# Kernel tuning notes

Measured on AMD Instinct MI355X. Metric: run time of the kernel, lower is better.

Reference implementation:

```python
import jax, jax.numpy as jnp
import numpy as np

# Dimensions: B batch, NAP/NUE node counts (= permutation_size1/2), DEG fixed degree,
# EAP/EUE edge counts, D1/D2 feature dims, OUT output_dim, S sample_size.
B, NAP, NUE, DEG = 64, 256, 128, 32
EAP, EUE = NAP * DEG, NUE * DEG
D1, D2, OUT, S = 64, 32, 64, 10
LOG2PI = float(np.log(2.0 * np.pi))


def setup_inputs() -> dict:
    ks = jax.random.split(jax.random.key(0), 16)

    def u(k, shape, fan):  # torch init: uniform(-sqrt(3/fan), sqrt(3/fan))
        ini = float(np.sqrt(3.0 / fan))
        return jax.random.uniform(k, shape, jnp.float32, -ini, ini)

    return {
        "A_AP": jax.random.normal(ks[0], (B, D1, NAP), jnp.float32),
        "A_UE": jax.random.normal(ks[1], (B, D1, NUE), jnp.float32),
        "H": jax.random.normal(ks[2], (B, D2, NAP, NUE), jnp.float32),
        "Q1_AP": u(ks[3], (2 * OUT, D1), OUT * 2 * D1),
        "Q2_AP": u(ks[4], (2 * OUT, D1), OUT * 2 * D1),
        "Q1_UE": u(ks[5], (2 * OUT, D1), OUT * 2 * D1),
        "Q2_UE": u(ks[6], (2 * OUT, D1), OUT * 2 * D1),
        "P1_AP": u(ks[7], (2 * OUT, D2), OUT * 2 * D2),
        "P1_UE": u(ks[8], (2 * OUT, D2), OUT * 2 * D2),
        "Att_AP": u(ks[9], (2 * D1, 1), D1 * 2),
        "Att_UE": u(ks[10], (2 * D1, 1), D1 * 2),
        "bn_weight": jnp.ones((2 * OUT,), jnp.float32),
        "bn_bias": jnp.zeros((2 * OUT,), jnp.float32),
        "Graph_AP_reshape": jax.random.randint(ks[11], (B, 2, EAP), 0, NAP),
        "Graph_UE_reshape": jax.random.randint(ks[12], (B, 2, EUE), 0, NUE),
        "GFA_AP": jax.random.randint(ks[13], (B, NAP, DEG), 0, EAP),
        "GFA_UE": jax.random.randint(ks[14], (B, NUE, DEG), 0, EUE),
        "permutation_size1": NAP,
        "permutation_size2": NUE,
        "BATCH_SIZE": B,
    }


def _gather_nodes(A, idx):
    # A: [B, D, N], idx: [B, E] -> [B, E, D]  (replaces the outer-product+diagonal trick)
    return jnp.take_along_axis(A, idx[:, None, :], axis=2).transpose(0, 2, 1)


def _neighbor_sampling(x_i, x_j, att, key):
    # x_i, x_j: [B, E, D]; att: [2D, 1]
    score = jnp.squeeze(jnp.concatenate([x_i, x_j], axis=-1) @ att, -1)  # [B, E]
    alpha = jnp.clip(jax.nn.sigmoid(jax.nn.leaky_relu(score, 0.2)), 0.01, 0.99)
    logits = jnp.log(alpha) - jnp.log1p(-alpha)
    noise = jax.random.logistic(key, alpha.shape, alpha.dtype)
    gate = jax.nn.sigmoid((logits + noise) / 0.1)  # RelaxedBernoulli(temp=0.1).rsample()
    return x_j * gate[..., None], alpha


def _agg_edges(edge_x, gfa):
    # edge_x: [B, E, D]; gfa: [B, N, deg] indices into E -> [B, D, N] (sum over deg)
    b, n, deg = gfa.shape
    g = jnp.take_along_axis(edge_x, gfa.reshape(b, n * deg, 1), axis=1)
    return g.reshape(b, n, deg, -1).sum(2).transpose(0, 2, 1)


def _kl_bern(a, p=0.5):
    # KL(Bernoulli(a) || Bernoulli(p)) summed over edges -> [B]
    return (a * (jnp.log(a) - jnp.log(p)) + (1 - a) * (jnp.log1p(-a) - jnp.log(1 - p))).sum(-1)


def _batchnorm(x, w, b, eps=1e-5):
    # BatchNorm1d (training-mode batch stats) on [B, C, N]
    m = x.mean(axis=(0, 2), keepdims=True)
    v = jnp.mean((x - m) ** 2, axis=(0, 2), keepdims=True)
    return (x - m) / jnp.sqrt(v + eps) * w[None, :, None] + b[None, :, None]


def _info_xz(A_r, key):
    # A_r: [M, 2*OUT]; diag-Gaussian reparam, S samples, KL-ish MC estimate -> [M]
    mean, raw = A_r[:, :OUT], A_r[:, OUT:]
    std = jax.nn.softplus(raw) + 1e-10
    eps = jax.random.normal(key, (S,) + mean.shape, mean.dtype)
    Z = mean + std * eps
    logq = (-0.5 * eps ** 2 - jnp.log(std) - 0.5 * LOG2PI).sum(-1)
    logp = (-0.5 * Z ** 2 - 0.5 * LOG2PI).sum(-1)
    return (logq - logp).mean(0)


def _forward(floats, Graph_AP_reshape, Graph_UE_reshape, GFA_AP, GFA_UE, p1, p2, bs):
    (A_AP, A_UE, H, Q1_AP, Q2_AP, Q1_UE, Q2_UE,
     P1_AP, P1_UE, Att_AP, Att_UE, bn_w, bn_b) = floats
    k1, k2, k3, k4 = jax.random.split(jax.random.key(42), 4)

    xi_ap = _gather_nodes(A_AP, Graph_AP_reshape[:, 1])
    xj_ap = _gather_nodes(A_AP, Graph_AP_reshape[:, 0])
    xi_ue = _gather_nodes(A_UE, Graph_UE_reshape[:, 1])
    xj_ue = _gather_nodes(A_UE, Graph_UE_reshape[:, 0])

    xj_ap, alpha_ap = _neighbor_sampling(xi_ap, xj_ap, Att_AP, k1)
    xj_ue, alpha_ue = _neighbor_sampling(xi_ue, xj_ue, Att_UE, k2)

    Aap = _agg_edges(xj_ap, GFA_AP)  # [B, D1, NAP]
    Aue = _agg_edges(xj_ue, GFA_UE)  # [B, D1, NUE]

    I_AZ_AP = _kl_bern(alpha_ap)
    I_AZ_UE = _kl_bern(alpha_ue)

    ap = (2.0 * jnp.einsum('od,bdn->bon', Q1_AP, Aap)
          + 2.0 * jnp.einsum('od,bd->bo', Q2_AP, Aue.mean(-1))[:, :, None]
          + 0.1 * jnp.einsum('od,bdn->bon', P1_AP, H.mean(-1)))
    ue = (2.0 * jnp.einsum('od,bdn->bon', Q1_UE, Aue)
          + 2.0 * jnp.einsum('od,bd->bo', Q2_UE, Aap.mean(-1))[:, :, None]
          + 0.1 * jnp.einsum('od,bdn->bon', P1_UE, H.mean(-2)))

    ap = _batchnorm(jax.nn.relu(ap), bn_w, bn_b)
    ue = _batchnorm(jax.nn.relu(ue), bn_w, bn_b)

    I_XZ_AP = _info_xz(ap.transpose(0, 2, 1).reshape(bs * p1, 2 * OUT), k3).reshape(bs, p1).sum(-1)
    I_XZ_UE = _info_xz(ue.transpose(0, 2, 1).reshape(bs * p2, 2 * OUT), k4).reshape(bs, p2).sum(-1)

    return ap[:, :OUT], ue[:, :OUT], I_XZ_AP, I_XZ_UE, I_AZ_AP, I_AZ_UE


def reference(A_AP, A_UE, H, Q1_AP, Q2_AP, Q1_UE, Q2_UE, P1_AP, P1_UE,
              Att_AP, Att_UE, bn_weight, bn_bias,
              Graph_AP_reshape, Graph_UE_reshape, GFA_AP, GFA_UE,
              permutation_size1, permutation_size2, BATCH_SIZE):
    floats = (A_AP, A_UE, H, Q1_AP, Q2_AP, Q1_UE, Q2_UE,
              P1_AP, P1_UE, Att_AP, Att_UE, bn_weight, bn_bias)
    return _forward(floats, Graph_AP_reshape, Graph_UE_reshape, GFA_AP, GFA_UE,
                    permutation_size1, permutation_size2, BATCH_SIZE)
```

## Files before the change

kernel.cpp:

```cpp
#include <hip/hip_runtime.h>
#include <math.h>

#define BB   64
#define NAP  256
#define NUE  128
#define DEG  32
#define EAP  (NAP*DEG)
#define EUE  (NUE*DEG)
#define D1   64
#define D2   32
#define OUTC 64
#define CH   128
#define SS   10

#define TINYF 1.17549435e-38f
#define LOG_HALF (-0.69314718f)

constexpr unsigned rotl_c(unsigned v, int s) { return (v << s) | (v >> (32 - s)); }
struct KeyPair { unsigned hi, lo; };
constexpr KeyPair tf_ck(unsigned k0, unsigned k1, unsigned x0, unsigned x1) {
  unsigned ks2 = k0 ^ k1 ^ 0x1BD11BDAu;
  x0 += k0; x1 += k1;
  const int R[20] = {13,15,26,6, 17,29,16,24, 13,15,26,6, 17,29,16,24, 13,15,26,6};
  const unsigned ia[5] = {k1, ks2, k0, k1, ks2};
  const unsigned ib[5] = {ks2, k0, k1, ks2, k0};
  for (int g = 0; g < 5; ++g) {
    for (int j = 0; j < 4; ++j) { x0 += x1; x1 = rotl_c(x1, R[g*4+j]); x1 ^= x0; }
    x0 += ia[g]; x1 += ib[g] + (unsigned)(g + 1);
  }
  return KeyPair{x0, x1};
}
constexpr KeyPair SK1 = tf_ck(0u, 42u, 0u, 0u);
constexpr KeyPair SK2 = tf_ck(0u, 42u, 0u, 1u);
constexpr KeyPair SK3 = tf_ck(0u, 42u, 0u, 2u);
constexpr KeyPair SK4 = tf_ck(0u, 42u, 0u, 3u);

__device__ __forceinline__ unsigned rb32(unsigned k0, unsigned k1, unsigned ctr) {
  const unsigned ks2 = k0 ^ k1 ^ 0x1BD11BDAu;
  unsigned x0 = k0;
  unsigned x1 = ctr + k1;
#define TFR(r) { x0 += x1; x1 = (x1 << r) | (x1 >> (32 - r)); x1 ^= x0; }
  TFR(13) TFR(15) TFR(26) TFR(6)
  x0 += k1;  x1 += ks2 + 1u;
  TFR(17) TFR(29) TFR(16) TFR(24)
  x0 += ks2; x1 += k0 + 2u;
  TFR(13) TFR(15) TFR(26) TFR(6)
  x0 += k0;  x1 += k1 + 3u;
  TFR(17) TFR(29) TFR(16) TFR(24)
  x0 += k1;  x1 += ks2 + 4u;
  TFR(13) TFR(15) TFR(26) TFR(6)
  x0 += ks2; x1 += k0 + 5u;
#undef TFR
  return x0 ^ x1;
}

__device__ __forceinline__ float bits_to_unit(unsigned bits) {
  return __uint_as_float((bits >> 9) | 0x3f800000u) - 1.0f;
}

__device__ __forceinline__ float erfinv_f32(float x) {
  float w = -log1pf(-x * x);
  float p;
  if (w < 5.0f) {
    w = w - 2.5f;
    p = 2.81022636e-08f;
    p = fmaf(p, w, 3.43273939e-07f);
    p = fmaf(p, w, -3.5233877e-06f);
    p = fmaf(p, w, -4.39150654e-06f);
    p = fmaf(p, w, 0.00021858087f);
    p = fmaf(p, w, -0.00125372503f);
    p = fmaf(p, w, -0.00417768164f);
    p = fmaf(p, w, 0.246640727f);
    p = fmaf(p, w, 1.50140941f);
  } else {
    w = sqrtf(w) - 3.0f;
    p = -0.000200214257f;
    p = fmaf(p, w, 0.000100950558f);
    p = fmaf(p, w, 0.00134934322f);
    p = fmaf(p, w, -0.00367342844f);
    p = fmaf(p, w, 0.00573950773f);
    p = fmaf(p, w, -0.0076224613f);
    p = fmaf(p, w, 0.00943887047f);
    p = fmaf(p, w, 1.00167406f);
    p = fmaf(p, w, 2.83297682f);
  }
  return p * x;
}

__device__ __forceinline__ float normal_from_bits(unsigned bits) {
  float f = bits_to_unit(bits);
  const float lo = -0.99999994f;
  float u = fmaxf(lo, fmaf(f, 2.0f, lo));
  return 1.41421354f * erfinv_f32(u);
}

__device__ __forceinline__ float softplus_f(float x) {
  return fmaxf(x, 0.0f) + log1pf(expf(-fabsf(x)));
}

__global__ __launch_bounds__(256) void edge_kernel(
    const float* __restrict__ A_AP, const float* __restrict__ A_UE,
    const int* __restrict__ GAP, const int* __restrict__ GUE,
    const float* __restrict__ AttAP, const float* __restrict__ AttUE,
    float* __restrict__ gAP, float* __restrict__ gUE,
    float* __restrict__ IAZ_AP, float* __restrict__ IAZ_UE,
    float* __restrict__ amAP, float* __restrict__ amUE)
{
  const int side = blockIdx.y;
  const int b = blockIdx.x;
  const int N = side ? NUE : NAP;
  const int E = side ? EUE : EAP;
  const float* A  = (side ? A_UE : A_AP) + (size_t)b * D1 * N;
  const int* G    = (side ? GUE : GAP) + (size_t)b * 2 * E;
  const float* At = side ? AttUE : AttAP;
  float* gate     = (side ? gUE : gAP) + (size_t)b * E;
  float* IAZ      = side ? IAZ_UE : IAZ_AP;
  float* am       = side ? amUE : amAP;
  const unsigned k0 = side ? SK2.hi : SK1.hi;
  const unsigned k1 = side ? SK2.lo : SK1.lo;
  const int t = threadIdx.x;

  if (t < D1) am[b * D1 + t] = 0.f;

  __shared__ float si_s[NAP];
  __shared__ float sj_s[NAP];
  if (t < N) {
    float a0 = 0.f, a1 = 0.f;
    #pragma unroll
    for (int d = 0; d < D1; ++d) {
      float v = A[d * N + t];
      a0 = fmaf(v, At[d], a0);
      a1 = fmaf(v, At[D1 + d], a1);
    }
    si_s[t] = a0; sj_s[t] = a1;
  }
  __syncthreads();

  float klacc = 0.f;
  for (int e = t; e < E; e += 256) {
    const int ii = G[E + e];
    const int jj = G[e];
    float score = si_s[ii] + sj_s[jj];
    float l = (score >= 0.f) ? score : 0.2f * score;
    float sig = 1.f / (1.f + expf(-l));
    float a = fminf(fmaxf(sig, 0.01f), 0.99f);
    float logits = logf(a) - log1pf(-a);
    unsigned bits = rb32(k0, k1, (unsigned)(b * E + e));
    float f = bits_to_unit(bits);
    float u = fmaxf(TINYF, f + TINYF);
    float noise = logf(u) - log1pf(-u);
    float gv = 1.f / (1.f + expf(-((logits + noise) / 0.1f)));
    gate[e] = gv;
    klacc += a * (logf(a) - LOG_HALF) + (1.f - a) * (log1pf(-a) - LOG_HALF);
  }
  #pragma unroll
  for (int m = 32; m; m >>= 1) klacc += __shfl_xor(klacc, m, 64);
  __shared__ float red[4];
  if ((t & 63) == 0) red[t >> 6] = klacc;
  __syncthreads();
  if (t == 0) IAZ[b] = red[0] + red[1] + red[2] + red[3];
}

template<int N, int E>
__global__ __launch_bounds__(256) void agg_kernel(
    const float* __restrict__ A, const int* __restrict__ Graph,
    const float* __restrict__ gate, const int* __restrict__ GFA,
    float* __restrict__ Aout, float* __restrict__ AmeanRaw)
{
  __shared__ float Als[D1 * N];
  const int b = blockIdx.y;
  const int t = threadIdx.x;
  const int wave = t >> 6, lane = t & 63;
  const int n = blockIdx.x * 64 + lane;

  const int* G0 = Graph + (size_t)b * 2 * E;
  const float* gb = gate + (size_t)b * E;
  const int* gfa = GFA + ((size_t)b * N + n) * DEG;
  int jj[DEG]; float gg[DEG];
  #pragma unroll
  for (int k = 0; k < DEG; ++k) {
    int e = gfa[k];
    jj[k] = G0[e];
    gg[k] = gb[e];
  }

  const float* Ab = A + (size_t)b * D1 * N;
  for (int idx = t * 4; idx < D1 * N; idx += 1024)
    *(float4*)(Als + idx) = *(const float4*)(Ab + idx);
  __syncthreads();

  for (int dd = 0; dd < 16; ++dd) {
    const int d = wave * 16 + dd;
    const float* Ar = Als + d * N;
    float acc = 0.f;
    #pragma unroll
    for (int k = 0; k < DEG; ++k) acc = fmaf(gg[k], Ar[jj[k]], acc);
    Aout[((size_t)b * D1 + d) * N + n] = acc;
    float s = acc;
    #pragma unroll
    for (int m = 32; m; m >>= 1) s += __shfl_xor(s, m, 64);
    if (lane == 0) atomicAdd(&AmeanRaw[b * D1 + d], s);
  }
}

__global__ __launch_bounds__(256) void hreduce_kernel(
    const float* __restrict__ H, float* __restrict__ Hm1, float* __restrict__ Hm2)
{
  const int bd = blockIdx.x;
  const float* Hp = H + (size_t)bd * NAP * NUE;
  const int t = threadIdx.x;
  const int tx = t & 31, ty = t >> 5;
  float4 col = {0.f, 0.f, 0.f, 0.f};
  for (int i = ty; i < NAP; i += 8) {
    float4 v = ((const float4*)(Hp + (size_t)i * NUE))[tx];
    col.x += v.x; col.y += v.y; col.z += v.z; col.w += v.w;
    float rs = v.x + v.y + v.z + v.w;
    #pragma unroll
    for (int m = 16; m; m >>= 1) rs += __shfl_xor(rs, m, 64);
    if (tx == 0) Hm1[(size_t)bd * NAP + i] = rs * (1.0f / NUE);
  }
  __shared__ float cp[8 * 128];
  ((float4*)cp)[ty * 32 + tx] = col;
  __syncthreads();
  if (t < 128) {
    float s = 0.f;
    #pragma unroll
    for (int r = 0; r < 8; ++r) s += cp[r * 128 + t];
    Hm2[(size_t)bd * NUE + t] = s * (1.0f / NAP);
  }
}

__global__ __launch_bounds__(128) void qterm_kernel(
    const float* __restrict__ Q2_AP, const float* __restrict__ Q2_UE,
    const float* __restrict__ AapMeanRaw, const float* __restrict__ AueMeanRaw,
    float* __restrict__ qbAP, float* __restrict__ qbUE,
    float* __restrict__ stAP, float* __restrict__ stUE)
{
  const int b = blockIdx.x;
  const int o = threadIdx.x;
  if (b == 0) {
    #pragma unroll
    for (int i = o; i < 2 * CH; i += 128) { stAP[i] = 0.f; stUE[i] = 0.f; }
  }
  float sA = 0.f, sU = 0.f;
  #pragma unroll
  for (int d = 0; d < D1; ++d) {
    float mUE = AueMeanRaw[b * D1 + d] * (1.0f / NUE);
    float mAP = AapMeanRaw[b * D1 + d] * (1.0f / NAP);
    sA = fmaf(Q2_AP[o * D1 + d], mUE, sA);
    sU = fmaf(Q2_UE[o * D1 + d], mAP, sU);
  }
  qbAP[b * CH + o] = 2.f * sA;
  qbUE[b * CH + o] = 2.f * sU;
}

__global__ __launch_bounds__(256) void mix_kernel(
    const float* __restrict__ Aagg, const float* __restrict__ Hm,
    const float* __restrict__ Q1, const float* __restrict__ P1,
    const float* __restrict__ qb, float* __restrict__ pre,
    float* __restrict__ stat, int N)
{
  const int b = blockIdx.z;
  const int ntile = blockIdx.x;
  const int obase = blockIdx.y * 8;
  __shared__ float As2[D1 * 128];
  __shared__ float Hs[D2 * 128];
  const int t = threadIdx.x;
  const float* Ab = Aagg + (size_t)b * D1 * N + ntile * 128;
  for (int idx = t; idx < D1 * 128; idx += 256) {
    int d = idx >> 7, n = idx & 127;
    As2[idx] = Ab[(size_t)d * N + n];
  }
  const float* Hb = Hm + (size_t)b * D2 * N + ntile * 128;
  for (int idx = t; idx < D2 * 128; idx += 256) {
    int c = idx >> 7, n = idx & 127;
    Hs[idx] = Hb[(size_t)c * N + n];
  }
  __syncthreads();
  const int half = t >> 7, n = t & 127;
  #pragma unroll
  for (int oi = 0; oi < 4; ++oi) {
    const int o = obase + half * 4 + oi;
    float acc = 0.f;
    #pragma unroll
    for (int d = 0; d < D1; ++d) acc = fmaf(Q1[o * D1 + d], As2[d * 128 + n], acc);
    float acc2 = 0.f;
    #pragma unroll
    for (int c = 0; c < D2; ++c) acc2 = fmaf(P1[o * D2 + c], Hs[c * 128 + n], acc2);
    float r = 2.f * acc + qb[b * CH + o] + 0.1f * acc2;
    r = fmaxf(r, 0.f);
    pre[((size_t)b * CH + o) * N + ntile * 128 + n] = r;
    float s1 = r, s2 = r * r;
    #pragma unroll
    for (int m = 32; m; m >>= 1) { s1 += __shfl_xor(s1, m, 64); s2 += __shfl_xor(s2, m, 64); }
    if ((t & 63) == 0) { atomicAdd(&stat[o], s1); atomicAdd(&stat[CH + o], s2); }
  }
}

__global__ __launch_bounds__(256) void bnfinal_kernel(
    const float* __restrict__ statAP, const float* __restrict__ statUE,
    const float* __restrict__ bnw, const float* __restrict__ bnb,
    float* __restrict__ ssAP, float* __restrict__ ssUE,
    float* __restrict__ IXZ)
{
  const int t = threadIdx.x;
  if (t < 2 * BB) IXZ[t] = 0.f;
  if (t < CH) {
    const float inv = 1.0f / (BB * NAP);
    float m = statAP[t] * inv;
    float v = statAP[CH + t] * inv - m * m;
    float sc = bnw[t] / sqrtf(v + 1e-5f);
    ssAP[t] = sc; ssAP[CH + t] = bnb[t] - m * sc;
  } else {
    const int o = t - CH;
    const float inv = 1.0f / (BB * NUE);
    float m = statUE[o] * inv;
    float v = statUE[CH + o] * inv - m * m;
    float sc = bnw[o] / sqrtf(v + 1e-5f);
    ssUE[o] = sc; ssUE[CH + o] = bnb[o] - m * sc;
  }
}

__global__ __launch_bounds__(256) void finalize_kernel(
    const float* __restrict__ preAP, const float* __restrict__ preUE,
    const float* __restrict__ ssAP, const float* __restrict__ ssUE,
    float* __restrict__ outAP, float* __restrict__ outUE,
    float* __restrict__ IXZAP, float* __restrict__ IXZUE)
{
  const int side = blockIdx.z;
  const int N = side ? NUE : NAP;
  if ((int)blockIdx.x * 64 >= N) return;
  const float* pre = side ? preUE : preAP;
  const float* ss  = side ? ssUE  : ssAP;
  float* outp      = side ? outUE : outAP;
  float* IXZ       = side ? IXZUE : IXZAP;
  const unsigned k0 = side ? SK4.hi : SK3.hi;
  const unsigned k1 = side ? SK4.lo : SK3.lo;
  const int ROWS = BB * N;

  const int b = blockIdx.y;
  const int lane = threadIdx.x & 63;
  const int og = threadIdx.x >> 6;
  const int n = blockIdx.x * 64 + lane;
  const int row = b * N + n;
  const float* preb = pre + (size_t)b * CH * N;

  float accZ = 0.f, sumlog = 0.f;
  for (int oi = 0; oi < 16; ++oi) {
    const int o = og * 16 + oi;
    float mpre = preb[o * N + n];
    float rraw = preb[(o + 64) * N + n];
    float x0 = fmaf(mpre, ss[o], ss[CH + o]);
    float x1 = fmaf(rraw, ss[o + 64], ss[CH + o + 64]);
    outp[((size_t)b * OUTC + o) * N + n] = x0;
    float stdv = softplus_f(x1) + 1e-10f;
    sumlog += logf(stdv);
    #pragma unroll
    for (int s = 0; s < SS; ++s) {
      unsigned idx = (unsigned)((s * ROWS + row) * 64 + o);
      float eps = normal_from_bits(rb32(k0, k1, idx));
      float Z = fmaf(stdv, eps, x0);
      accZ += 0.5f * (Z * Z - eps * eps);
    }
  }
  __shared__ float pz[4][64];
  __shared__ float pl[4][64];
  pz[og][lane] = accZ; pl[og][lane] = sumlog;
  __syncthreads();
  if (og == 0) {
    float az = pz[0][lane] + pz[1][lane] + pz[2][lane] + pz[3][lane];
    float al = pl[0][lane] + pl[1][lane] + pl[2][lane] + pl[3][lane];
    float rv = az * (1.0f / SS) - al;
    #pragma unroll
    for (int m = 32; m; m >>= 1) rv += __shfl_xor(rv, m, 64);
    if (lane == 0) atomicAdd(&IXZ[b], rv);
  }
}

constexpr size_t OFF_AMEAN_AP = 0;
constexpr size_t OFF_AMEAN_UE = OFF_AMEAN_AP + BB * D1;
constexpr size_t OFF_STAT_AP  = OFF_AMEAN_UE + BB * D1;
constexpr size_t OFF_STAT_UE  = OFF_STAT_AP + 2 * CH;
constexpr size_t OFF_GATE_AP  = OFF_STAT_UE + 2 * CH;
constexpr size_t OFF_GATE_UE  = OFF_GATE_AP + (size_t)BB * EAP;
constexpr size_t OFF_AAP      = OFF_GATE_UE + (size_t)BB * EUE;
constexpr size_t OFF_AUE      = OFF_AAP + (size_t)BB * D1 * NAP;
constexpr size_t OFF_HM1      = OFF_AUE + (size_t)BB * D1 * NUE;
constexpr size_t OFF_HM2      = OFF_HM1 + (size_t)BB * D2 * NAP;
constexpr size_t OFF_PRE_AP   = OFF_HM2 + (size_t)BB * D2 * NUE;
constexpr size_t OFF_PRE_UE   = OFF_PRE_AP + (size_t)BB * CH * NAP;
constexpr size_t OFF_QB_AP    = OFF_PRE_UE + (size_t)BB * CH * NUE;
constexpr size_t OFF_QB_UE    = OFF_QB_AP + BB * CH;
constexpr size_t OFF_SS_AP    = OFF_QB_UE + BB * CH;
constexpr size_t OFF_SS_UE    = OFF_SS_AP + 2 * CH;
constexpr size_t WS_FLOATS    = OFF_SS_UE + 2 * CH;

extern "C" void kernel_launch(void* const* d_in, const int* in_sizes, int n_in,
                              void* d_out, int out_size, void* d_ws, size_t ws_size,
                              hipStream_t stream)
{
  const float* A_AP  = (const float*)d_in[0];
  const float* A_UE  = (const float*)d_in[1];
  const float* H     = (const float*)d_in[2];
  const float* Q1_AP = (const float*)d_in[3];
  const float* Q2_AP = (const float*)d_in[4];
  const float* Q1_UE = (const float*)d_in[5];
  const float* Q2_UE = (const float*)d_in[6];
  const float* P1_AP = (const float*)d_in[7];
  const float* P1_UE = (const float*)d_in[8];
  const float* AttAP = (const float*)d_in[9];
  const float* AttUE = (const float*)d_in[10];
  const float* bnw   = (const float*)d_in[11];
  const float* bnb   = (const float*)d_in[12];
  const int* GraphAP = (const int*)d_in[13];
  const int* GraphUE = (const int*)d_in[14];
  const int* GFA_AP  = (const int*)d_in[15];
  const int* GFA_UE  = (const int*)d_in[16];

  float* ws = (float*)d_ws;
  if (ws_size < WS_FLOATS * sizeof(float)) return;

  float* amAP  = ws + OFF_AMEAN_AP;
  float* amUE  = ws + OFF_AMEAN_UE;
  float* stAP  = ws + OFF_STAT_AP;
  float* stUE  = ws + OFF_STAT_UE;
  float* gAP   = ws + OFF_GATE_AP;
  float* gUE   = ws + OFF_GATE_UE;
  float* Aap   = ws + OFF_AAP;
  float* Aue   = ws + OFF_AUE;
  float* Hm1   = ws + OFF_HM1;
  float* Hm2   = ws + OFF_HM2;
  float* preAP = ws + OFF_PRE_AP;
  float* preUE = ws + OFF_PRE_UE;
  float* qbAP  = ws + OFF_QB_AP;
  float* qbUE  = ws + OFF_QB_UE;
  float* ssAP  = ws + OFF_SS_AP;
  float* ssUE  = ws + OFF_SS_UE;

  float* out     = (float*)d_out;
  float* outAP   = out;
  float* outUE   = out + (size_t)BB * OUTC * NAP;
  float* IXZ_AP  = out + (size_t)BB * OUTC * (NAP + NUE);
  float* IXZ_UE  = IXZ_AP + BB;
  float* IAZ_AP  = IXZ_UE + BB;
  float* IAZ_UE  = IAZ_AP + BB;

  edge_kernel<<<dim3(BB, 2), 256, 0, stream>>>(
      A_AP, A_UE, GraphAP, GraphUE, AttAP, AttUE,
      gAP, gUE, IAZ_AP, IAZ_UE, amAP, amUE);

  hreduce_kernel<<<BB * D2, 256, 0, stream>>>(H, Hm1, Hm2);

  agg_kernel<NAP, EAP><<<dim3(NAP / 64, BB), 256, 0, stream>>>(
      A_AP, GraphAP, gAP, GFA_AP, Aap, amAP);
  agg_kernel<NUE, EUE><<<dim3(NUE / 64, BB), 256, 0, stream>>>(
      A_UE, GraphUE, gUE, GFA_UE, Aue, amUE);

  qterm_kernel<<<BB, 128, 0, stream>>>(Q2_AP, Q2_UE, amAP, amUE, qbAP, qbUE, stAP, stUE);

  mix_kernel<<<dim3(NAP / 128, 16, BB), 256, 0, stream>>>(
      Aap, Hm1, Q1_AP, P1_AP, qbAP, preAP, stAP, NAP);
  mix_kernel<<<dim3(NUE / 128, 16, BB), 256, 0, stream>>>(
      Aue, Hm2, Q1_UE, P1_UE, qbUE, preUE, stUE, NUE);

  bnfinal_kernel<<<1, 256, 0, stream>>>(stAP, stUE, bnw, bnb, ssAP, ssUE, IXZ_AP);

  finalize_kernel<<<dim3(NAP / 64, BB, 2), 256, 0, stream>>>(
      preAP, preUE, ssAP, ssUE, outAP, outUE, IXZ_AP, IXZ_UE);
}
```

Measured before the change: 778.5 us.

## Merge AP/UE launches and register-tile the mix GEMM over all channels

Fuses the AP and UE agg launches into one grid and likewise for mix, cutting launch count. The mix kernel is restructured so each block covers all 128 output channels for a 64-node tile, with weights staged in padded shared memory and each thread computing an 8x4 register tile. This removes the repeated reloading of A/H tiles across 16 channel-group blocks and the global weight reads, and lowers atomic traffic. It also adds an unroll pragma to the H reduction loop. The cost is higher shared memory and register use per block, which may reduce occupancy.

```diff
diff --git a/kernel.cpp b/kernel.cpp
--- a/kernel.cpp
+++ b/kernel.cpp
@@ -161,21 +161,32 @@
   if (t == 0) IAZ[b] = red[0] + red[1] + red[2] + red[3];
 }
 
-template<int N, int E>
 __global__ __launch_bounds__(256) void agg_kernel(
-    const float* __restrict__ A, const int* __restrict__ Graph,
-    const float* __restrict__ gate, const int* __restrict__ GFA,
-    float* __restrict__ Aout, float* __restrict__ AmeanRaw)
-{
-  __shared__ float Als[D1 * N];
+    const float* __restrict__ A_AP, const float* __restrict__ A_UE,
+    const int* __restrict__ GAP, const int* __restrict__ GUE,
+    const float* __restrict__ gAP, const float* __restrict__ gUE,
+    const int* __restrict__ GFA_AP, const int* __restrict__ GFA_UE,
+    float* __restrict__ Aap, float* __restrict__ Aue,
+    float* __restrict__ amAP, float* __restrict__ amUE)
+{
+  __shared__ float Als[D1 * NAP];
+  const int x = blockIdx.x;
+  const int side = (x >= NAP / 64);
+  const int tile = side ? x - NAP / 64 : x;
   const int b = blockIdx.y;
+  const int N = side ? NUE : NAP;
+  const int E = side ? EUE : EAP;
+  const float* A  = (side ? A_UE : A_AP) + (size_t)b * D1 * N;
+  const int* G0   = (side ? GUE : GAP) + (size_t)b * 2 * E;
+  const float* gb = (side ? gUE : gAP) + (size_t)b * E;
+  float* Aout = side ? Aue : Aap;
+  float* am   = side ? amUE : amAP;
+
   const int t = threadIdx.x;
   const int wave = t >> 6, lane = t & 63;
-  const int n = blockIdx.x * 64 + lane;
-
-  const int* G0 = Graph + (size_t)b * 2 * E;
-  const float* gb = gate + (size_t)b * E;
-  const int* gfa = GFA + ((size_t)b * N + n) * DEG;
+  const int n = tile * 64 + lane;
+
+  const int* gfa = (side ? GFA_UE : GFA_AP) + ((size_t)b * N + n) * DEG;
   int jj[DEG]; float gg[DEG];
   #pragma unroll
   for (int k = 0; k < DEG; ++k) {
@@ -184,9 +195,8 @@
     gg[k] = gb[e];
   }
 
-  const float* Ab = A + (size_t)b * D1 * N;
   for (int idx = t * 4; idx < D1 * N; idx += 1024)
-    *(float4*)(Als + idx) = *(const float4*)(Ab + idx);
+    *(float4*)(Als + idx) = *(const float4*)(A + idx);
   __syncthreads();
 
   for (int dd = 0; dd < 16; ++dd) {
@@ -199,7 +209,7 @@
     float s = acc;
     #pragma unroll
     for (int m = 32; m; m >>= 1) s += __shfl_xor(s, m, 64);
-    if (lane == 0) atomicAdd(&AmeanRaw[b * D1 + d], s);
+    if (lane == 0) atomicAdd(&am[b * D1 + d], s);
   }
 }
 
@@ -211,6 +221,7 @@
   const int t = threadIdx.x;
   const int tx = t & 31, ty = t >> 5;
   float4 col = {0.f, 0.f, 0.f, 0.f};
+  #pragma unroll 4
   for (int i = ty; i < NAP; i += 8) {
     float4 v = ((const float4*)(Hp + (size_t)i * NUE))[tx];
     col.x += v.x; col.y += v.y; col.z += v.z; col.w += v.w;
@@ -255,45 +266,78 @@
 }
 
 __global__ __launch_bounds__(256) void mix_kernel(
-    const float* __restrict__ Aagg, const float* __restrict__ Hm,
-    const float* __restrict__ Q1, const float* __restrict__ P1,
-    const float* __restrict__ qb, float* __restrict__ pre,
-    float* __restrict__ stat, int N)
-{
-  const int b = blockIdx.z;
-  const int ntile = blockIdx.x;
-  const int obase = blockIdx.y * 8;
-  __shared__ float As2[D1 * 128];
-  __shared__ float Hs[D2 * 128];
+    const float* __restrict__ Aap, const float* __restrict__ Aue,
+    const float* __restrict__ Hm1, const float* __restrict__ Hm2,
+    const float* __restrict__ Q1_AP, const float* __restrict__ Q1_UE,
+    const float* __restrict__ P1_AP, const float* __restrict__ P1_UE,
+    const float* __restrict__ qbAP, const float* __restrict__ qbUE,
+    float* __restrict__ preAP, float* __restrict__ preUE,
+    float* __restrict__ stAP, float* __restrict__ stUE)
+{
+  __shared__ float Qs[CH * 65];
+  __shared__ float Ps[CH * 33];
+  __shared__ float As[D1 * 64];
+  __shared__ float Hs[D2 * 64];
+  const int x = blockIdx.x;
+  const int side = (x >= NAP / 64);
+  const int tile = side ? x - NAP / 64 : x;
+  const int b = blockIdx.y;
+  const int N = side ? NUE : NAP;
+  const float* Aagg = (side ? Aue : Aap) + (size_t)b * D1 * N + tile * 64;
+  const float* Hm   = (side ? Hm2 : Hm1) + (size_t)b * D2 * N + tile * 64;
+  const float* Q1   = side ? Q1_UE : Q1_AP;
+  const float* P1   = side ? P1_UE : P1_AP;
+  const float* qb   = (side ? qbUE : qbAP) + b * CH;
+  float* pre        = (side ? preUE : preAP) + (size_t)b * CH * N + tile * 64;
+  float* stat       = side ? stUE : stAP;
+
   const int t = threadIdx.x;
-  const float* Ab = Aagg + (size_t)b * D1 * N + ntile * 128;
-  for (int idx = t; idx < D1 * 128; idx += 256) {
-    int d = idx >> 7, n = idx & 127;
-    As2[idx] = Ab[(size_t)d * N + n];
-  }
-  const float* Hb = Hm + (size_t)b * D2 * N + ntile * 128;
-  for (int idx = t; idx < D2 * 128; idx += 256) {
-    int c = idx >> 7, n = idx & 127;
-    Hs[idx] = Hb[(size_t)c * N + n];
-  }
+  for (int i = t; i < CH * D1; i += 256) Qs[(i >> 6) * 65 + (i & 63)] = Q1[i];
+  for (int i = t; i < CH * D2; i += 256) Ps[(i >> 5) * 33 + (i & 31)] = P1[i];
+  for (int i = t; i < D1 * 64; i += 256) As[i] = Aagg[(size_t)(i >> 6) * N + (i & 63)];
+  for (int i = t; i < D2 * 64; i += 256) Hs[i] = Hm[(size_t)(i >> 6) * N + (i & 63)];
   __syncthreads();
-  const int half = t >> 7, n = t & 127;
+
+  const int tn = t & 15, to = t >> 4;
+  float accQ[8][4] = {};
+  for (int d = 0; d < D1; ++d) {
+    float4 a = *(const float4*)&As[d * 64 + tn * 4];
+    #pragma unroll
+    for (int oi = 0; oi < 8; ++oi) {
+      float w = Qs[(to * 8 + oi) * 65 + d];
+      accQ[oi][0] = fmaf(w, a.x, accQ[oi][0]);
+      accQ[oi][1] = fmaf(w, a.y, accQ[oi][1]);
+      accQ[oi][2] = fmaf(w, a.z, accQ[oi][2]);
+      accQ[oi][3] = fmaf(w, a.w, accQ[oi][3]);
+    }
+  }
+  float accP[8][4] = {};
+  for (int c = 0; c < D2; ++c) {
+    float4 h = *(const float4*)&Hs[c * 64 + tn * 4];
+    #pragma unroll
+    for (int oi = 0; oi < 8; ++oi) {
+      float w = Ps[(to * 8 + oi) * 33 + c];
+      accP[oi][0] = fmaf(w, h.x, accP[oi][0]);
+      accP[oi][1] = fmaf(w, h.y, accP[oi][1]);
+      accP[oi][2] = fmaf(w, h.z, accP[oi][2]);
+      accP[oi][3] = fmaf(w, h.w, accP[oi][3]);
+    }
+  }
   #pragma unroll
-  for (int oi = 0; oi < 4; ++oi) {
-    const int o = obase + half * 4 + oi;
-    float acc = 0.f;
-    #pragma unroll
-    for (int d = 0; d < D1; ++d) acc = fmaf(Q1[o * D1 + d], As2[d * 128 + n], acc);
-    float acc2 = 0.f;
-    #pragma unroll
-    for (int c = 0; c < D2; ++c) acc2 = fmaf(P1[o * D2 + c], Hs[c * 128 + n], acc2);
-    float r = 2.f * acc + qb[b * CH + o] + 0.1f * acc2;
-    r = fmaxf(r, 0.f);
-    pre[((size_t)b * CH + o) * N + ntile * 128 + n] = r;
-    float s1 = r, s2 = r * r;
-    #pragma unroll
-    for (int m = 32; m; m >>= 1) { s1 += __shfl_xor(s1, m, 64); s2 += __shfl_xor(s2, m, 64); }
-    if ((t & 63) == 0) { atomicAdd(&stat[o], s1); atomicAdd(&stat[CH + o], s2); }
+  for (int oi = 0; oi < 8; ++oi) {
+    const int o = to * 8 + oi;
+    const float base = qb[o];
+    float4 r;
+    r.x = fmaxf(2.f * accQ[oi][0] + base + 0.1f * accP[oi][0], 0.f);
+    r.y = fmaxf(2.f * accQ[oi][1] + base + 0.1f * accP[oi][1], 0.f);
+    r.z = fmaxf(2.f * accQ[oi][2] + base + 0.1f * accP[oi][2], 0.f);
+    r.w = fmaxf(2.f * accQ[oi][3] + base + 0.1f * accP[oi][3], 0.f);
+    *(float4*)&pre[(size_t)o * N + tn * 4] = r;
+    float s1 = r.x + r.y + r.z + r.w;
+    float s2 = r.x * r.x + r.y * r.y + r.z * r.z + r.w * r.w;
+    #pragma unroll
+    for (int m = 1; m < 16; m <<= 1) { s1 += __shfl_xor(s1, m, 64); s2 += __shfl_xor(s2, m, 64); }
+    if (tn == 0) { atomicAdd(&stat[o], s1); atomicAdd(&stat[CH + o], s2); }
   }
 }
 
@@ -451,17 +495,15 @@
 
   hreduce_kernel<<<BB * D2, 256, 0, stream>>>(H, Hm1, Hm2);
 
-  agg_kernel<NAP, EAP><<<dim3(NAP / 64, BB), 256, 0, stream>>>(
-      A_AP, GraphAP, gAP, GFA_AP, Aap, amAP);
-  agg_kernel<NUE, EUE><<<dim3(NUE / 64, BB), 256, 0, stream>>>(
-      A_UE, GraphUE, gUE, GFA_UE, Aue, amUE);
+  agg_kernel<<<dim3(NAP / 64 + NUE / 64, BB), 256, 0, stream>>>(
+      A_AP, A_UE, GraphAP, GraphUE, gAP, gUE, GFA_AP, GFA_UE,
+      Aap, Aue, amAP, amUE);
 
   qterm_kernel<<<BB, 128, 0, stream>>>(Q2_AP, Q2_UE, amAP, amUE, qbAP, qbUE, stAP, stUE);
 
-  mix_kernel<<<dim3(NAP / 128, 16, BB), 256, 0, stream>>>(
-      Aap, Hm1, Q1_AP, P1_AP, qbAP, preAP, stAP, NAP);
-  mix_kernel<<<dim3(NUE / 128, 16, BB), 256, 0, stream>>>(
-      Aue, Hm2, Q1_UE, P1_UE, qbUE, preUE, stUE, NUE);
+  mix_kernel<<<dim3(NAP / 64 + NUE / 64, BB), 256, 0, stream>>>(
+      Aap, Aue, Hm1, Hm2, Q1_AP, Q1_UE, P1_AP, P1_UE,
+      qbAP, qbUE, preAP, preUE, stAP, stUE);
 
   bnfinal_kernel<<<1, 256, 0, stream>>>(stAP, stUE, bnw, bnb, ssAP, ssUE, IXZ_AP);
 
```

Result: faster. 669.1 us (-14.1%).
